# Optimization experiments

Measured on AMD Instinct MI355X. Metric: run time of the kernel, lower is better.

The kernel has to match this reference:

```python
import jax, jax.numpy as jnp
import numpy as np

NUM_GRAPHS = 256
NUM_LAYERS = 4
HIDDEN = 256
N_FEATS = 9
VOCAB = 119
BN_EPS = 1e-5


def setup_inputs() -> dict:
    key = jax.random.key(0)
    ks = jax.random.split(key, 16)
    N, E, H = 10000, 320000, HIDDEN
    x = jax.random.randint(ks[0], (N, N_FEATS), 0, 2, dtype=jnp.int64)
    edge_index = jax.random.randint(ks[1], (2, E), 0, N, dtype=jnp.int64)
    batch_ids = jnp.sort(jax.random.randint(ks[2], (N,), 0, NUM_GRAPHS, dtype=jnp.int64))
    s = 1.0 / np.sqrt(H)
    emb = jax.random.normal(ks[3], (N_FEATS, VOCAB, H), jnp.float32) * 0.02
    W = jax.random.normal(ks[4], (NUM_LAYERS, H, H), jnp.float32) * s
    b = jnp.zeros((NUM_LAYERS, H), jnp.float32)
    gamma = jnp.ones((NUM_LAYERS, H), jnp.float32)
    beta = jnp.zeros((NUM_LAYERS, H), jnp.float32)
    mlp_W1 = jax.random.normal(ks[5], (H, H // 2), jnp.float32) * s
    mlp_b1 = jnp.zeros((H // 2,), jnp.float32)
    mlp_W2 = jax.random.normal(ks[6], (H // 2, H // 4), jnp.float32) * (1.0 / np.sqrt(H // 2))
    mlp_b2 = jnp.zeros((H // 4,), jnp.float32)
    mlp_W3 = jax.random.normal(ks[7], (H // 4, 1), jnp.float32) * (1.0 / np.sqrt(H // 4))
    mlp_b3 = jnp.zeros((1,), jnp.float32)
    return dict(x=x, edge_index=edge_index, batch_ids=batch_ids, emb=emb, W=W, b=b,
                gamma=gamma, beta=beta, mlp_W1=mlp_W1, mlp_b1=mlp_b1,
                mlp_W2=mlp_W2, mlp_b2=mlp_b2, mlp_W3=mlp_W3, mlp_b3=mlp_b3)


def reference(x, edge_index, batch_ids, emb, W, b, gamma, beta,
              mlp_W1, mlp_b1, mlp_W2, mlp_b2, mlp_W3, mlp_b3):
    N = x.shape[0]
    src, dst = edge_index[0], edge_index[1]

    # AtomEncoder: sum of per-feature embeddings. emb[f, x[:,f]] -> [N, 9, H]
    h = jnp.sum(emb[jnp.arange(N_FEATS), x], axis=1)

    # GCN normalization with self-loops: deg_i = 1 + in-degree, norm = deg^-1/2
    deg = 1.0 + jax.ops.segment_sum(jnp.ones_like(dst, jnp.float32), dst, num_segments=N)
    nrm = jax.lax.rsqrt(deg)
    edge_w = (nrm[src] * nrm[dst])[:, None]   # [E,1]
    self_w = (nrm * nrm)[:, None]             # [N,1]

    for l in range(NUM_LAYERS):
        identity = h
        hw = h @ W[l]                                     # dense GEMM [N,H]x[H,H]
        agg = jax.ops.segment_sum(hw[src] * edge_w, dst, num_segments=N) + hw * self_w
        h = agg + b[l]
        # BatchNorm1d (training statistics over nodes)
        mu = jnp.mean(h, axis=0)
        var = jnp.var(h, axis=0)
        h = (h - mu) * jax.lax.rsqrt(var + BN_EPS) * gamma[l] + beta[l]
        h = jax.nn.relu(h)
        h = h + identity  # residual

    # global mean pool over graph ids
    sums = jax.ops.segment_sum(h, batch_ids, num_segments=NUM_GRAPHS)
    cnt = jax.ops.segment_sum(jnp.ones((N,), jnp.float32), batch_ids, num_segments=NUM_GRAPHS)
    g = sums / jnp.maximum(cnt, 1.0)[:, None]             # [G, H]

    # MLP head [H, H/2, H/4, 1]
    g = jax.nn.relu(g @ mlp_W1 + mlp_b1)
    g = jax.nn.relu(g @ mlp_W2 + mlp_b2)
    return g @ mlp_W3 + mlp_b3
```

## Files before the change

### kernel.cpp

```cpp
#include <hip/hip_runtime.h>

#define HID 256
#define NFEAT 9
#define VOCAB 119
#define NLAYERS 4
#define NGRAPHS 256
#define BN_EPS 1e-5f

typedef short short8 __attribute__((ext_vector_type(8)));
typedef float floatx4 __attribute__((ext_vector_type(4)));

__device__ inline unsigned short f2bf(float f) {
    unsigned int u = __float_as_uint(f);
    unsigned int r = u + 0x7FFF + ((u >> 16) & 1);
    return (unsigned short)(r >> 16);
}
__device__ inline float bf2f(unsigned short u) {
    return __uint_as_float(((unsigned int)u) << 16);
}

__global__ __launch_bounds__(256) void setup_misc(
        const int* __restrict__ x, const float* __restrict__ emb,
        const float* __restrict__ W,
        int* __restrict__ degi, int* __restrict__ fillc, float* __restrict__ bnsums,
        unsigned short* __restrict__ wt, unsigned short* __restrict__ hbA,
        int N, int zb) {
    const int bx = blockIdx.x;
    const int tid = threadIdx.x;
    __shared__ float sw[32][33];
    __shared__ int xf[NFEAT];

    if (bx < zb) {
        int i = bx * 256 + tid;
        if (i < N) { degi[i] = 0; fillc[i] = 0; }
        if (bx == 0) {
            for (int j = tid; j < NLAYERS * 2 * HID; j += 256) bnsums[j] = 0.f;
        }
    } else if (bx < zb + 256) {
        int j = bx - zb;
        int l = j >> 6;
        int rem = j & 63;
        int k0 = (rem >> 3) * 32, n0 = (rem & 7) * 32;
        int c = tid & 31, r8 = tid >> 5;
        const float* Wl = W + (size_t)l * HID * HID;
        unsigned short* Wtl = wt + (size_t)l * HID * HID;
#pragma unroll
        for (int p = 0; p < 4; ++p) {
            int r = r8 + p * 8;
            sw[r][c] = Wl[(k0 + r) * HID + n0 + c];
        }
        __syncthreads();
#pragma unroll
        for (int p = 0; p < 4; ++p) {
            int r = r8 + p * 8;
            Wtl[(size_t)(n0 + r) * HID + k0 + c] = f2bf(sw[c][r]);
        }
    } else {
        int n = bx - zb - 256;
        if (n < N) {
            if (tid < NFEAT) xf[tid] = x[n * NFEAT + tid];
            __syncthreads();
            float s = 0.f;
#pragma unroll
            for (int f = 0; f < NFEAT; ++f) s += emb[(size_t)(f * VOCAB + xf[f]) * HID + tid];
            hbA[(size_t)n * HID + tid] = f2bf(s);
        }
    }
}

__global__ void deg_kernel(const int* __restrict__ dst, int* __restrict__ degi, int E) {
    int i = blockIdx.x * blockDim.x + threadIdx.x;
    if (i < E) atomicAdd(&degi[dst[i]], 1);
}

__global__ __launch_bounds__(1024) void scan_kernel(const int* __restrict__ degi,
                                                    int* __restrict__ row_ptr,
                                                    float* __restrict__ nrm, int N) {
    int tid = threadIdx.x;
    int ch = (N + 1023) >> 10;
    int i0 = tid * ch;
    int i1 = min(i0 + ch, N);
    if (i0 > N) i0 = N;
    int local = 0;
    for (int i = i0; i < i1; ++i) local += degi[i];
    int lane = tid & 63, wid = tid >> 6;
    int v = local;
#pragma unroll
    for (int off = 1; off < 64; off <<= 1) {
        int u = __shfl_up(v, off);
        if (lane >= off) v += u;
    }
    __shared__ int wsum[16];
    if (lane == 63) wsum[wid] = v;
    __syncthreads();
    if (tid < 16) {
        int w = wsum[tid];
#pragma unroll
        for (int off = 1; off < 16; off <<= 1) {
            int u = __shfl_up(w, off);
            if (tid >= off) w += u;
        }
        wsum[tid] = w;
    }
    __syncthreads();
    int base = (wid > 0 ? wsum[wid - 1] : 0) + (v - local);
    int run = base;
    for (int i = i0; i < i1; ++i) {
        int d = degi[i];
        row_ptr[i] = run;
        run += d;
        nrm[i] = rsqrtf(1.0f + (float)d);
    }
    if (tid == 0) row_ptr[N] = wsum[15];
}

__global__ void fill_kernel(const int* __restrict__ src, const int* __restrict__ dst,
                            const int* __restrict__ row_ptr, int* __restrict__ fill,
                            const float* __restrict__ nrm,
                            int2* __restrict__ edges, int E) {
    int i = blockIdx.x * blockDim.x + threadIdx.x;
    if (i < E) {
        int d = dst[i];
        int s = src[i];
        int pos = row_ptr[d] + atomicAdd(&fill[d], 1);
        int2 rec;
        rec.x = s;
        rec.y = __float_as_int(nrm[s] * nrm[d]);
        edges[pos] = rec;
    }
}

__global__ __launch_bounds__(256) void agg_w8_kernel(const unsigned short* __restrict__ hb,
                                                     const int* __restrict__ row_ptr,
                                                     const int2* __restrict__ edges,
                                                     const float* __restrict__ nrm,
                                                     unsigned short* __restrict__ aggb, int N) {
    int tid = threadIdx.x;
    int wave = tid >> 6;
    int lane = tid & 63;
    int sub = lane >> 5;
    int sl = lane & 31;
    int n = blockIdx.x * 4 + wave;
    if (n >= N) return;
    int co = sl * 8;
    int s = row_ptr[n], e = row_ptr[n + 1];
    int len = e - s;
    int h0 = (len + 1) >> 1;
    int base = s + sub * h0;
    int cnt = sub ? (len - h0) : h0;
    float a[8];
#pragma unroll
    for (int j = 0; j < 8; ++j) a[j] = 0.f;
    int it = 0;
    for (; it + 3 < cnt; it += 4) {
        int2 e0 = edges[base + it];
        int2 e1 = edges[base + it + 1];
        int2 e2 = edges[base + it + 2];
        int2 e3 = edges[base + it + 3];
        short8 u0 = *(const short8*)&hb[(size_t)e0.x * HID + co];
        short8 u1 = *(const short8*)&hb[(size_t)e1.x * HID + co];
        short8 u2 = *(const short8*)&hb[(size_t)e2.x * HID + co];
        short8 u3 = *(const short8*)&hb[(size_t)e3.x * HID + co];
        float w0 = __int_as_float(e0.y);
        float w1 = __int_as_float(e1.y);
        float w2 = __int_as_float(e2.y);
        float w3 = __int_as_float(e3.y);
#pragma unroll
        for (int j = 0; j < 8; ++j)
            a[j] += w0 * bf2f((unsigned short)u0[j]) + w1 * bf2f((unsigned short)u1[j])
                  + w2 * bf2f((unsigned short)u2[j]) + w3 * bf2f((unsigned short)u3[j]);
    }
    for (; it < cnt; ++it) {
        int2 e0 = edges[base + it];
        short8 u0 = *(const short8*)&hb[(size_t)e0.x * HID + co];
        float w0 = __int_as_float(e0.y);
#pragma unroll
        for (int j = 0; j < 8; ++j) a[j] += w0 * bf2f((unsigned short)u0[j]);
    }
#pragma unroll
    for (int j = 0; j < 8; ++j) a[j] += __shfl_xor(a[j], 32);
    if (sub == 0) {
        float nd = nrm[n];
        float sw2 = nd * nd;
        short8 us = *(const short8*)&hb[(size_t)n * HID + co];
        short8 o;
#pragma unroll
        for (int j = 0; j < 8; ++j) {
            float v = a[j] + sw2 * bf2f((unsigned short)us[j]);
            o[j] = (short)f2bf(v);
        }
        *(short8*)&aggb[(size_t)n * HID + co] = o;
    }
}

__global__ __launch_bounds__(256) void mfma_gemm128(const unsigned short* __restrict__ A,
                                                    const unsigned short* __restrict__ Bt,
                                                    const float* __restrict__ bias,
                                                    unsigned short* __restrict__ C,
                                                    float* __restrict__ sums, int M) {
    __shared__ unsigned short As[128][40];
    __shared__ unsigned short Bs[64][40];
    __shared__ float lsum[64];
    __shared__ float lsq[64];
    int tid = threadIdx.x;
    int row0 = blockIdx.x * 128;
    int col0 = blockIdx.y * 64;
    int lane = tid & 63;
    int wid = tid >> 6;
    int arow = tid >> 1;
    int akc = (tid & 1) * 16;
    int brow = tid >> 2;
    int bkc = (tid & 3) * 8;
    int wm = (wid & 1) * 64;
    int wn = (wid >> 1) * 32;
    int quad = lane >> 4;
    int ln = lane & 15;

    floatx4 acc[4][2];
#pragma unroll
    for (int r = 0; r < 4; ++r)
#pragma unroll
        for (int c = 0; c < 2; ++c) acc[r][c] = (floatx4){0.f, 0.f, 0.f, 0.f};

    if (tid < 64) { lsum[tid] = 0.f; lsq[tid] = 0.f; }

    for (int kk = 0; kk < HID; kk += 32) {
        short8 av0 = {0, 0, 0, 0, 0, 0, 0, 0};
        short8 av1 = {0, 0, 0, 0, 0, 0, 0, 0};
        int ar = row0 + arow;
        if (ar < M) {
            av0 = *(const short8*)&A[(size_t)ar * HID + kk + akc];
            av1 = *(const short8*)&A[(size_t)ar * HID + kk + akc + 8];
        }
        short8 bv = *(const short8*)&Bt[(size_t)(col0 + brow) * HID + kk + bkc];
        *(short8*)&As[arow][akc] = av0;
        *(short8*)&As[arow][akc + 8] = av1;
        *(short8*)&Bs[brow][bkc] = bv;
        __syncthreads();
        short8 bf0 = *(const short8*)&Bs[wn + ln][quad * 8];
        short8 bf1 = *(const short8*)&Bs[wn + 16 + ln][quad * 8];
#pragma unroll
        for (int r = 0; r < 4; ++r) {
            short8 af = *(const short8*)&As[wm + r * 16 + ln][quad * 8];
            acc[r][0] = __builtin_amdgcn_mfma_f32_16x16x32_bf16(af, bf0, acc[r][0], 0, 0, 0);
            acc[r][1] = __builtin_amdgcn_mfma_f32_16x16x32_bf16(af, bf1, acc[r][1], 0, 0, 0);
        }
        __syncthreads();
    }
    float bias0 = bias[col0 + wn + ln];
    float bias1 = bias[col0 + wn + 16 + ln];
    float p0 = 0.f, q0 = 0.f, p1 = 0.f, q1 = 0.f;
#pragma unroll
    for (int r = 0; r < 4; ++r) {
#pragma unroll
        for (int rr = 0; rr < 4; ++rr) {
            int row = row0 + wm + r * 16 + quad * 4 + rr;
            if (row < M) {
                float v0 = acc[r][0][rr] + bias0;
                float v1 = acc[r][1][rr] + bias1;
                C[(size_t)row * HID + col0 + wn + ln] = f2bf(v0);
                C[(size_t)row * HID + col0 + wn + 16 + ln] = f2bf(v1);
                p0 += v0; q0 += v0 * v0;
                p1 += v1; q1 += v1 * v1;
            }
        }
    }
    atomicAdd(&lsum[wn + ln], p0);
    atomicAdd(&lsq[wn + ln], q0);
    atomicAdd(&lsum[wn + 16 + ln], p1);
    atomicAdd(&lsq[wn + 16 + ln], q1);
    __syncthreads();
    if (tid < 64) {
        unsafeAtomicAdd(&sums[col0 + tid], lsum[tid]);
        unsafeAtomicAdd(&sums[HID + col0 + tid], lsq[tid]);
    }
}

__global__ __launch_bounds__(256) void bn_kernel(const unsigned short* __restrict__ hwb,
                                                 const float* __restrict__ sums,
                                                 const float* __restrict__ gamma,
                                                 const float* __restrict__ beta,
                                                 const unsigned short* __restrict__ hold,
                                                 unsigned short* __restrict__ hbnew, int N) {
    int i4 = blockIdx.x * blockDim.x + threadIdx.x;
    int base = i4 * 4;
    if (base >= N * HID) return;
    int c = base & (HID - 1);
    float invN = 1.0f / (float)N;
    float4 s4 = *(const float4*)&sums[c];
    float4 q4 = *(const float4*)&sums[HID + c];
    float4 g4 = *(const float4*)&gamma[c];
    float4 be4 = *(const float4*)&beta[c];
    ushort4 v = *(const ushort4*)&hwb[base];
    ushort4 r = *(const ushort4*)&hold[base];
    ushort4 o;
    {
        float mu = s4.x * invN, var = q4.x * invN - mu * mu;
        o.x = f2bf(fmaxf((bf2f(v.x) - mu) * g4.x * rsqrtf(var + BN_EPS) + be4.x, 0.f) + bf2f(r.x));
        mu = s4.y * invN; var = q4.y * invN - mu * mu;
        o.y = f2bf(fmaxf((bf2f(v.y) - mu) * g4.y * rsqrtf(var + BN_EPS) + be4.y, 0.f) + bf2f(r.y));
        mu = s4.z * invN; var = q4.z * invN - mu * mu;
        o.z = f2bf(fmaxf((bf2f(v.z) - mu) * g4.z * rsqrtf(var + BN_EPS) + be4.z, 0.f) + bf2f(r.z));
        mu = s4.w * invN; var = q4.w * invN - mu * mu;
        o.w = f2bf(fmaxf((bf2f(v.w) - mu) * g4.w * rsqrtf(var + BN_EPS) + be4.w, 0.f) + bf2f(r.w));
    }
    *(ushort4*)&hbnew[base] = o;
}

__device__ inline int lower_bound_g(const int* __restrict__ a, int n, int key) {
    int lo = 0, hi = n;
    while (lo < hi) {
        int mid = (lo + hi) >> 1;
        if (a[mid] < key) lo = mid + 1; else hi = mid;
    }
    return lo;
}

__global__ __launch_bounds__(256) void pool_mlp_bn_kernel(
        const unsigned short* __restrict__ hwb,
        const float* __restrict__ sums,
        const float* __restrict__ gamma,
        const float* __restrict__ beta,
        const unsigned short* __restrict__ resid,
        const int* __restrict__ batch, int N,
        const float* __restrict__ W1, const float* __restrict__ b1,
        const float* __restrict__ W2, const float* __restrict__ b2,
        const float* __restrict__ W3, const float* __restrict__ b3,
        float* __restrict__ out) {
    int g = blockIdx.x, tid = threadIdx.x;
    int lo = lower_bound_g(batch, N, g);
    int hi = lower_bound_g(batch, N, g + 1);
    float invN = 1.0f / (float)N;
    float mu = sums[tid] * invN;
    float var = sums[HID + tid] * invN - mu * mu;
    float sc = gamma[tid] * rsqrtf(var + BN_EPS);
    float be = beta[tid];
    float s = 0.f;
    for (int i = lo; i < hi; ++i) {
        float v = (bf2f(hwb[(size_t)i * HID + tid]) - mu) * sc + be;
        v = fmaxf(v, 0.f) + bf2f(resid[(size_t)i * HID + tid]);
        s += v;
    }
    __shared__ float gs[256];
    __shared__ float t1[128];
    __shared__ float t2[64];
    float inv = 1.0f / fmaxf((float)(hi - lo), 1.0f);
    gs[tid] = s * inv;
    __syncthreads();
    if (tid < 128) {
        float a = b1[tid];
        for (int k = 0; k < 256; ++k) a += gs[k] * W1[k * 128 + tid];
        t1[tid] = fmaxf(a, 0.f);
    }
    __syncthreads();
    if (tid < 64) {
        float a = b2[tid];
        for (int k = 0; k < 128; ++k) a += t1[k] * W2[k * 64 + tid];
        t2[tid] = fmaxf(a, 0.f);
    }
    __syncthreads();
    if (tid < 64) {
        float p = t2[tid] * W3[tid];
#pragma unroll
        for (int off = 32; off >= 1; off >>= 1) p += __shfl_down(p, off);
        if (tid == 0) out[g] = p + b3[0];
    }
}

extern "C" void kernel_launch(void* const* d_in, const int* in_sizes, int n_in,
                              void* d_out, int out_size, void* d_ws, size_t ws_size,
                              hipStream_t stream) {
    const int* x      = (const int*)d_in[0];
    const int* ei     = (const int*)d_in[1];
    const int* batch  = (const int*)d_in[2];
    const float* emb  = (const float*)d_in[3];
    const float* W    = (const float*)d_in[4];
    const float* b    = (const float*)d_in[5];
    const float* gamma= (const float*)d_in[6];
    const float* beta = (const float*)d_in[7];
    const float* W1   = (const float*)d_in[8];
    const float* b1   = (const float*)d_in[9];
    const float* W2   = (const float*)d_in[10];
    const float* b2   = (const float*)d_in[11];
    const float* W3   = (const float*)d_in[12];
    const float* b3   = (const float*)d_in[13];
    float* out = (float*)d_out;

    int N = in_sizes[0] / NFEAT;
    int E = in_sizes[1] / 2;
    const int* srcp = ei;
    const int* dstp = ei + E;

    char* ws = (char*)d_ws;
    auto alloc = [&](size_t bytes) -> char* {
        char* p = ws;
        ws += (bytes + 255) & ~(size_t)255;
        return p;
    };
    int* degi     = (int*)alloc((size_t)N * 4);
    int* row_ptr  = (int*)alloc((size_t)(N + 1) * 4);
    int* fillc    = (int*)alloc((size_t)N * 4);
    float* nrm    = (float*)alloc((size_t)N * 4);
    int2* edges   = (int2*)alloc((size_t)E * 8);
    unsigned short* hbA  = (unsigned short*)alloc((size_t)N * HID * 2);
    unsigned short* hbB  = (unsigned short*)alloc((size_t)N * HID * 2);
    unsigned short* aggb = (unsigned short*)alloc((size_t)N * HID * 2);
    unsigned short* hwb  = (unsigned short*)alloc((size_t)N * HID * 2);
    unsigned short* wt   = (unsigned short*)alloc((size_t)NLAYERS * HID * HID * 2);
    float* bnsums = (float*)alloc((size_t)NLAYERS * 2 * HID * 4);

    int zb = (N + 255) / 256;
    int miscGrid = zb + 256 + N;
    setup_misc<<<miscGrid, 256, 0, stream>>>(x, emb, W, degi, fillc, bnsums, wt, hbA, N, zb);
    deg_kernel<<<(E + 255) / 256, 256, 0, stream>>>(dstp, degi, E);
    scan_kernel<<<1, 1024, 0, stream>>>(degi, row_ptr, nrm, N);
    fill_kernel<<<(E + 255) / 256, 256, 0, stream>>>(srcp, dstp, row_ptr, fillc, nrm, edges, E);

    unsigned short* hbcur = hbA;
    unsigned short* hboth = hbB;
    for (int l = 0; l < NLAYERS; ++l) {
        float* lsums = bnsums + (size_t)l * 2 * HID;
        agg_w8_kernel<<<(N + 3) / 4, 256, 0, stream>>>(hbcur, row_ptr, edges, nrm, aggb, N);
        dim3 ggrid((N + 127) / 128, 4);
        mfma_gemm128<<<ggrid, 256, 0, stream>>>(aggb, wt + (size_t)l * HID * HID,
                                                b + (size_t)l * HID, hwb, lsums, N);
        if (l < NLAYERS - 1) {
            bn_kernel<<<((size_t)N * HID / 4 + 255) / 256, 256, 0, stream>>>(
                hwb, lsums, gamma + (size_t)l * HID, beta + (size_t)l * HID,
                hbcur, hboth, N);
            unsigned short* tb = hbcur; hbcur = hboth; hboth = tb;
        }
    }

    pool_mlp_bn_kernel<<<NGRAPHS, 256, 0, stream>>>(
        hwb, bnsums + (size_t)3 * 2 * HID, gamma + (size_t)3 * HID, beta + (size_t)3 * HID,
        hbcur, batch, N, W1, b1, W2, b2, W3, b3, out);
}
```

Before: 304.0 us.

## Fuse BatchNorm into GEMM via grid barrier and shuffle-broadcast edge records

The separate BatchNorm/ReLU/residual kernel is folded into the GEMM epilogue. Each column-block group waits on a global atomic counter barrier until all row blocks have added their column statistics, then normalizes the accumulators still held in registers. This saves a full write and reread of the pre-BN activations and one launch per layer. The catch is that the spin barrier only works if all ~79x4 blocks are co-resident. Separately, the aggregation kernel now loads up to 32 edge records at once across lanes and broadcasts them with shuffles, instead of every lane reloading the same records.

```diff
diff --git a/kernel.cpp b/kernel.cpp
--- a/kernel.cpp
+++ b/kernel.cpp
@@ -18,11 +18,18 @@
 __device__ inline float bf2f(unsigned short u) {
     return __uint_as_float(((unsigned int)u) << 16);
 }
+__device__ inline unsigned int agent_load_u(const unsigned int* p) {
+    return __hip_atomic_load(p, __ATOMIC_RELAXED, __HIP_MEMORY_SCOPE_AGENT);
+}
+__device__ inline float agent_load_f(const float* p) {
+    return __hip_atomic_load(p, __ATOMIC_RELAXED, __HIP_MEMORY_SCOPE_AGENT);
+}
 
 __global__ __launch_bounds__(256) void setup_misc(
         const int* __restrict__ x, const float* __restrict__ emb,
         const float* __restrict__ W,
         int* __restrict__ degi, int* __restrict__ fillc, float* __restrict__ bnsums,
+        unsigned int* __restrict__ ctr,
         unsigned short* __restrict__ wt, unsigned short* __restrict__ hbA,
         int N, int zb) {
     const int bx = blockIdx.x;
@@ -35,6 +42,7 @@
         if (i < N) { degi[i] = 0; fillc[i] = 0; }
         if (bx == 0) {
             for (int j = tid; j < NLAYERS * 2 * HID; j += 256) bnsums[j] = 0.f;
+            if (tid < 16) ctr[tid] = 0u;
         }
     } else if (bx < zb + 256) {
         int j = bx - zb;
@@ -130,11 +138,11 @@
     }
 }
 
-__global__ __launch_bounds__(256) void agg_w8_kernel(const unsigned short* __restrict__ hb,
-                                                     const int* __restrict__ row_ptr,
-                                                     const int2* __restrict__ edges,
-                                                     const float* __restrict__ nrm,
-                                                     unsigned short* __restrict__ aggb, int N) {
+__global__ __launch_bounds__(256) void agg_shfl_kernel(const unsigned short* __restrict__ hb,
+                                                       const int* __restrict__ row_ptr,
+                                                       const int2* __restrict__ edges,
+                                                       const float* __restrict__ nrm,
+                                                       unsigned short* __restrict__ aggb, int N) {
     int tid = threadIdx.x;
     int wave = tid >> 6;
     int lane = tid & 63;
@@ -151,31 +159,32 @@
     float a[8];
 #pragma unroll
     for (int j = 0; j < 8; ++j) a[j] = 0.f;
-    int it = 0;
-    for (; it + 3 < cnt; it += 4) {
-        int2 e0 = edges[base + it];
-        int2 e1 = edges[base + it + 1];
-        int2 e2 = edges[base + it + 2];
-        int2 e3 = edges[base + it + 3];
-        short8 u0 = *(const short8*)&hb[(size_t)e0.x * HID + co];
-        short8 u1 = *(const short8*)&hb[(size_t)e1.x * HID + co];
-        short8 u2 = *(const short8*)&hb[(size_t)e2.x * HID + co];
-        short8 u3 = *(const short8*)&hb[(size_t)e3.x * HID + co];
-        float w0 = __int_as_float(e0.y);
-        float w1 = __int_as_float(e1.y);
-        float w2 = __int_as_float(e2.y);
-        float w3 = __int_as_float(e3.y);
-#pragma unroll
-        for (int j = 0; j < 8; ++j)
-            a[j] += w0 * bf2f((unsigned short)u0[j]) + w1 * bf2f((unsigned short)u1[j])
-                  + w2 * bf2f((unsigned short)u2[j]) + w3 * bf2f((unsigned short)u3[j]);
-    }
-    for (; it < cnt; ++it) {
-        int2 e0 = edges[base + it];
-        short8 u0 = *(const short8*)&hb[(size_t)e0.x * HID + co];
-        float w0 = __int_as_float(e0.y);
-#pragma unroll
-        for (int j = 0; j < 8; ++j) a[j] += w0 * bf2f((unsigned short)u0[j]);
+
+    int done = 0;
+    while (done < cnt) {
+        int m = min(32, cnt - done);
+        int li = done + (sl < m ? sl : m - 1);
+        int2 rec = edges[base + li];
+        int j = 0;
+        for (; j + 1 < m; j += 2) {
+            int s0 = __shfl(rec.x, j, 32);
+            int s1 = __shfl(rec.x, j + 1, 32);
+            float w0 = __int_as_float(__shfl(rec.y, j, 32));
+            float w1 = __int_as_float(__shfl(rec.y, j + 1, 32));
+            short8 u0 = *(const short8*)&hb[(size_t)s0 * HID + co];
+            short8 u1 = *(const short8*)&hb[(size_t)s1 * HID + co];
+#pragma unroll
+            for (int k = 0; k < 8; ++k)
+                a[k] += w0 * bf2f((unsigned short)u0[k]) + w1 * bf2f((unsigned short)u1[k]);
+        }
+        if (j < m) {
+            int s0 = __shfl(rec.x, j, 32);
+            float w0 = __int_as_float(__shfl(rec.y, j, 32));
+            short8 u0 = *(const short8*)&hb[(size_t)s0 * HID + co];
+#pragma unroll
+            for (int k = 0; k < 8; ++k) a[k] += w0 * bf2f((unsigned short)u0[k]);
+        }
+        done += m;
     }
 #pragma unroll
     for (int j = 0; j < 8; ++j) a[j] += __shfl_xor(a[j], 32);
@@ -197,7 +206,12 @@
                                                     const unsigned short* __restrict__ Bt,
                                                     const float* __restrict__ bias,
                                                     unsigned short* __restrict__ C,
-                                                    float* __restrict__ sums, int M) {
+                                                    float* __restrict__ sums,
+                                                    unsigned int* __restrict__ ctr,
+                                                    const unsigned short* __restrict__ resid,
+                                                    const float* __restrict__ gamma,
+                                                    const float* __restrict__ beta,
+                                                    int doBn, int M) {
     __shared__ unsigned short As[128][40];
     __shared__ unsigned short Bs[64][40];
     __shared__ float lsum[64];
@@ -247,8 +261,10 @@
         }
         __syncthreads();
     }
-    float bias0 = bias[col0 + wn + ln];
-    float bias1 = bias[col0 + wn + 16 + ln];
+    int c0 = col0 + wn + ln;
+    int c1 = col0 + wn + 16 + ln;
+    float bias0 = bias[c0];
+    float bias1 = bias[c1];
     float p0 = 0.f, q0 = 0.f, p1 = 0.f, q1 = 0.f;
 #pragma unroll
     for (int r = 0; r < 4; ++r) {
@@ -258,8 +274,12 @@
             if (row < M) {
                 float v0 = acc[r][0][rr] + bias0;
                 float v1 = acc[r][1][rr] + bias1;
-                C[(size_t)row * HID + col0 + wn + ln] = f2bf(v0);
-                C[(size_t)row * HID + col0 + wn + 16 + ln] = f2bf(v1);
+                acc[r][0][rr] = v0;
+                acc[r][1][rr] = v1;
+                if (!doBn) {
+                    C[(size_t)row * HID + c0] = f2bf(v0);
+                    C[(size_t)row * HID + c1] = f2bf(v1);
+                }
                 p0 += v0; q0 += v0 * v0;
                 p1 += v1; q1 += v1 * v1;
             }
@@ -274,37 +294,45 @@
         unsafeAtomicAdd(&sums[col0 + tid], lsum[tid]);
         unsafeAtomicAdd(&sums[HID + col0 + tid], lsq[tid]);
     }
-}
-
-__global__ __launch_bounds__(256) void bn_kernel(const unsigned short* __restrict__ hwb,
-                                                 const float* __restrict__ sums,
-                                                 const float* __restrict__ gamma,
-                                                 const float* __restrict__ beta,
-                                                 const unsigned short* __restrict__ hold,
-                                                 unsigned short* __restrict__ hbnew, int N) {
-    int i4 = blockIdx.x * blockDim.x + threadIdx.x;
-    int base = i4 * 4;
-    if (base >= N * HID) return;
-    int c = base & (HID - 1);
-    float invN = 1.0f / (float)N;
-    float4 s4 = *(const float4*)&sums[c];
-    float4 q4 = *(const float4*)&sums[HID + c];
-    float4 g4 = *(const float4*)&gamma[c];
-    float4 be4 = *(const float4*)&beta[c];
-    ushort4 v = *(const ushort4*)&hwb[base];
-    ushort4 r = *(const ushort4*)&hold[base];
-    ushort4 o;
-    {
-        float mu = s4.x * invN, var = q4.x * invN - mu * mu;
-        o.x = f2bf(fmaxf((bf2f(v.x) - mu) * g4.x * rsqrtf(var + BN_EPS) + be4.x, 0.f) + bf2f(r.x));
-        mu = s4.y * invN; var = q4.y * invN - mu * mu;
-        o.y = f2bf(fmaxf((bf2f(v.y) - mu) * g4.y * rsqrtf(var + BN_EPS) + be4.y, 0.f) + bf2f(r.y));
-        mu = s4.z * invN; var = q4.z * invN - mu * mu;
-        o.z = f2bf(fmaxf((bf2f(v.z) - mu) * g4.z * rsqrtf(var + BN_EPS) + be4.z, 0.f) + bf2f(r.z));
-        mu = s4.w * invN; var = q4.w * invN - mu * mu;
-        o.w = f2bf(fmaxf((bf2f(v.w) - mu) * g4.w * rsqrtf(var + BN_EPS) + be4.w, 0.f) + bf2f(r.w));
-    }
-    *(ushort4*)&hbnew[base] = o;
+    if (!doBn) return;
+
+    unsigned int* myctr = &ctr[blockIdx.y];
+    unsigned int target = gridDim.x;
+    __syncthreads();
+    if (tid == 0) {
+        __threadfence();
+        atomicAdd(myctr, 1u);
+        for (int k = 0; k < (1 << 22); ++k) {
+            if (agent_load_u(myctr) >= target) break;
+            __builtin_amdgcn_s_sleep(2);
+        }
+    }
+    __syncthreads();
+    __threadfence();
+    float invN = 1.0f / (float)M;
+    float mu0 = agent_load_f(&sums[c0]) * invN;
+    float vr0 = agent_load_f(&sums[HID + c0]) * invN - mu0 * mu0;
+    float mu1 = agent_load_f(&sums[c1]) * invN;
+    float vr1 = agent_load_f(&sums[HID + c1]) * invN - mu1 * mu1;
+    float sc0 = gamma[c0] * rsqrtf(vr0 + BN_EPS);
+    float sc1 = gamma[c1] * rsqrtf(vr1 + BN_EPS);
+    float be0 = beta[c0];
+    float be1 = beta[c1];
+#pragma unroll
+    for (int r = 0; r < 4; ++r) {
+#pragma unroll
+        for (int rr = 0; rr < 4; ++rr) {
+            int row = row0 + wm + r * 16 + quad * 4 + rr;
+            if (row < M) {
+                float v0 = fmaxf((acc[r][0][rr] - mu0) * sc0 + be0, 0.f)
+                         + bf2f(resid[(size_t)row * HID + c0]);
+                float v1 = fmaxf((acc[r][1][rr] - mu1) * sc1 + be1, 0.f)
+                         + bf2f(resid[(size_t)row * HID + c1]);
+                C[(size_t)row * HID + c0] = f2bf(v0);
+                C[(size_t)row * HID + c1] = f2bf(v1);
+            }
+        }
+    }
 }
 
 __device__ inline int lower_bound_g(const int* __restrict__ a, int n, int key) {
@@ -408,10 +436,11 @@
     unsigned short* hwb  = (unsigned short*)alloc((size_t)N * HID * 2);
     unsigned short* wt   = (unsigned short*)alloc((size_t)NLAYERS * HID * HID * 2);
     float* bnsums = (float*)alloc((size_t)NLAYERS * 2 * HID * 4);
+    unsigned int* ctr = (unsigned int*)alloc(16 * 4);
 
     int zb = (N + 255) / 256;
     int miscGrid = zb + 256 + N;
-    setup_misc<<<miscGrid, 256, 0, stream>>>(x, emb, W, degi, fillc, bnsums, wt, hbA, N, zb);
+    setup_misc<<<miscGrid, 256, 0, stream>>>(x, emb, W, degi, fillc, bnsums, ctr, wt, hbA, N, zb);
     deg_kernel<<<(E + 255) / 256, 256, 0, stream>>>(dstp, degi, E);
     scan_kernel<<<1, 1024, 0, stream>>>(degi, row_ptr, nrm, N);
     fill_kernel<<<(E + 255) / 256, 256, 0, stream>>>(srcp, dstp, row_ptr, fillc, nrm, edges, E);
@@ -420,15 +449,18 @@
     unsigned short* hboth = hbB;
     for (int l = 0; l < NLAYERS; ++l) {
         float* lsums = bnsums + (size_t)l * 2 * HID;
-        agg_w8_kernel<<<(N + 3) / 4, 256, 0, stream>>>(hbcur, row_ptr, edges, nrm, aggb, N);
+        agg_shfl_kernel<<<(N + 3) / 4, 256, 0, stream>>>(hbcur, row_ptr, edges, nrm, aggb, N);
         dim3 ggrid((N + 127) / 128, 4);
-        mfma_gemm128<<<ggrid, 256, 0, stream>>>(aggb, wt + (size_t)l * HID * HID,
-                                                b + (size_t)l * HID, hwb, lsums, N);
         if (l < NLAYERS - 1) {
-            bn_kernel<<<((size_t)N * HID / 4 + 255) / 256, 256, 0, stream>>>(
-                hwb, lsums, gamma + (size_t)l * HID, beta + (size_t)l * HID,
-                hbcur, hboth, N);
+            mfma_gemm128<<<ggrid, 256, 0, stream>>>(
+                aggb, wt + (size_t)l * HID * HID, b + (size_t)l * HID,
+                hboth, lsums, ctr + l * 4, hbcur,
+                gamma + (size_t)l * HID, beta + (size_t)l * HID, 1, N);
             unsigned short* tb = hbcur; hbcur = hboth; hboth = tb;
+        } else {
+            mfma_gemm128<<<ggrid, 256, 0, stream>>>(
+                aggb, wt + (size_t)l * HID * HID, b + (size_t)l * HID,
+                hwb, lsums, nullptr, nullptr, nullptr, nullptr, 0, N);
         }
     }
 
```

Result: slower. 412.8 us (+35.8%).

## Fuse neighbor aggregation with the weight GEMM into one kernel

Applied to the files above, without the earlier changes.

Merges the sparse aggregation kernel and the MFMA GEMM into a single kernel. Each block aggregates 16 node rows directly into shared memory, then multiplies them by the full 256x256 weight matrix, streamed through LDS in k-chunks, and applies bias and BN statistics. This removes the intermediate aggregated buffer round-trip through global memory and one launch per layer. In exchange, every block reloads the whole weight matrix for only 16 rows, and the number of global atomics on the BN sums grows.

```diff
diff --git a/kernel.cpp b/kernel.cpp
--- a/kernel.cpp
+++ b/kernel.cpp
@@ -130,150 +130,125 @@
     }
 }
 
-__global__ __launch_bounds__(256) void agg_w8_kernel(const unsigned short* __restrict__ hb,
-                                                     const int* __restrict__ row_ptr,
-                                                     const int2* __restrict__ edges,
-                                                     const float* __restrict__ nrm,
-                                                     unsigned short* __restrict__ aggb, int N) {
+__global__ __launch_bounds__(256) void agg_gemm(const unsigned short* __restrict__ hb,
+                                                const int* __restrict__ row_ptr,
+                                                const int2* __restrict__ edges,
+                                                const float* __restrict__ nrm,
+                                                const unsigned short* __restrict__ Bt,
+                                                const float* __restrict__ bias,
+                                                unsigned short* __restrict__ C,
+                                                float* __restrict__ sums, int N) {
+    __shared__ unsigned short As[16][264];
+    __shared__ unsigned short Bs[256][40];
+    __shared__ float lsum[256];
+    __shared__ float lsq[256];
     int tid = threadIdx.x;
     int wave = tid >> 6;
     int lane = tid & 63;
     int sub = lane >> 5;
     int sl = lane & 31;
-    int n = blockIdx.x * 4 + wave;
-    if (n >= N) return;
-    int co = sl * 8;
-    int s = row_ptr[n], e = row_ptr[n + 1];
-    int len = e - s;
-    int h0 = (len + 1) >> 1;
-    int base = s + sub * h0;
-    int cnt = sub ? (len - h0) : h0;
-    float a[8];
-#pragma unroll
-    for (int j = 0; j < 8; ++j) a[j] = 0.f;
-    int it = 0;
-    for (; it + 3 < cnt; it += 4) {
-        int2 e0 = edges[base + it];
-        int2 e1 = edges[base + it + 1];
-        int2 e2 = edges[base + it + 2];
-        int2 e3 = edges[base + it + 3];
-        short8 u0 = *(const short8*)&hb[(size_t)e0.x * HID + co];
-        short8 u1 = *(const short8*)&hb[(size_t)e1.x * HID + co];
-        short8 u2 = *(const short8*)&hb[(size_t)e2.x * HID + co];
-        short8 u3 = *(const short8*)&hb[(size_t)e3.x * HID + co];
-        float w0 = __int_as_float(e0.y);
-        float w1 = __int_as_float(e1.y);
-        float w2 = __int_as_float(e2.y);
-        float w3 = __int_as_float(e3.y);
-#pragma unroll
-        for (int j = 0; j < 8; ++j)
-            a[j] += w0 * bf2f((unsigned short)u0[j]) + w1 * bf2f((unsigned short)u1[j])
-                  + w2 * bf2f((unsigned short)u2[j]) + w3 * bf2f((unsigned short)u3[j]);
-    }
-    for (; it < cnt; ++it) {
-        int2 e0 = edges[base + it];
-        short8 u0 = *(const short8*)&hb[(size_t)e0.x * HID + co];
-        float w0 = __int_as_float(e0.y);
-#pragma unroll
-        for (int j = 0; j < 8; ++j) a[j] += w0 * bf2f((unsigned short)u0[j]);
-    }
-#pragma unroll
-    for (int j = 0; j < 8; ++j) a[j] += __shfl_xor(a[j], 32);
-    if (sub == 0) {
-        float nd = nrm[n];
-        float sw2 = nd * nd;
-        short8 us = *(const short8*)&hb[(size_t)n * HID + co];
-        short8 o;
-#pragma unroll
-        for (int j = 0; j < 8; ++j) {
-            float v = a[j] + sw2 * bf2f((unsigned short)us[j]);
-            o[j] = (short)f2bf(v);
-        }
-        *(short8*)&aggb[(size_t)n * HID + co] = o;
-    }
-}
-
-__global__ __launch_bounds__(256) void mfma_gemm128(const unsigned short* __restrict__ A,
-                                                    const unsigned short* __restrict__ Bt,
-                                                    const float* __restrict__ bias,
-                                                    unsigned short* __restrict__ C,
-                                                    float* __restrict__ sums, int M) {
-    __shared__ unsigned short As[128][40];
-    __shared__ unsigned short Bs[64][40];
-    __shared__ float lsum[64];
-    __shared__ float lsq[64];
-    int tid = threadIdx.x;
-    int row0 = blockIdx.x * 128;
-    int col0 = blockIdx.y * 64;
-    int lane = tid & 63;
-    int wid = tid >> 6;
-    int arow = tid >> 1;
-    int akc = (tid & 1) * 16;
-    int brow = tid >> 2;
-    int bkc = (tid & 3) * 8;
-    int wm = (wid & 1) * 64;
-    int wn = (wid >> 1) * 32;
+    int row0 = blockIdx.x * 16;
+
+    for (int q = 0; q < 4; ++q) {
+        int lr = wave * 4 + q;
+        int n = row0 + lr;
+        float a[8];
+#pragma unroll
+        for (int j = 0; j < 8; ++j) a[j] = 0.f;
+        if (n < N) {
+            int s = row_ptr[n], e = row_ptr[n + 1];
+            int len = e - s;
+            int h0 = (len + 1) >> 1;
+            int base = s + sub * h0;
+            int cnt = sub ? (len - h0) : h0;
+            int co = sl * 8;
+            int it = 0;
+            for (; it + 3 < cnt; it += 4) {
+                int2 e0 = edges[base + it];
+                int2 e1 = edges[base + it + 1];
+                int2 e2 = edges[base + it + 2];
+                int2 e3 = edges[base + it + 3];
+                short8 u0 = *(const short8*)&hb[(size_t)e0.x * HID + co];
+                short8 u1 = *(const short8*)&hb[(size_t)e1.x * HID + co];
+                short8 u2 = *(const short8*)&hb[(size_t)e2.x * HID + co];
+                short8 u3 = *(const short8*)&hb[(size_t)e3.x * HID + co];
+                float w0 = __int_as_float(e0.y);
+                float w1 = __int_as_float(e1.y);
+                float w2 = __int_as_float(e2.y);
+                float w3 = __int_as_float(e3.y);
+#pragma unroll
+                for (int j = 0; j < 8; ++j)
+                    a[j] += w0 * bf2f((unsigned short)u0[j]) + w1 * bf2f((unsigned short)u1[j])
+                          + w2 * bf2f((unsigned short)u2[j]) + w3 * bf2f((unsigned short)u3[j]);
+            }
+            for (; it < cnt; ++it) {
+                int2 e0 = edges[base + it];
+                short8 u0 = *(const short8*)&hb[(size_t)e0.x * HID + co];
+                float w0 = __int_as_float(e0.y);
+#pragma unroll
+                for (int j = 0; j < 8; ++j) a[j] += w0 * bf2f((unsigned short)u0[j]);
+            }
+#pragma unroll
+            for (int j = 0; j < 8; ++j) a[j] += __shfl_xor(a[j], 32);
+            if (sub == 0) {
+                float nd = nrm[n];
+                float sw2 = nd * nd;
+                short8 us = *(const short8*)&hb[(size_t)n * HID + co];
+                short8 o;
+#pragma unroll
+                for (int j = 0; j < 8; ++j) o[j] = (short)f2bf(a[j] + sw2 * bf2f((unsigned short)us[j]));
+                *(short8*)&As[lr][sl * 8] = o;
+            }
+        } else if (sub == 0) {
+            short8 z = {0, 0, 0, 0, 0, 0, 0, 0};
+            *(short8*)&As[lr][sl * 8] = z;
+        }
+    }
+    lsum[tid] = 0.f;
+    lsq[tid] = 0.f;
+    __syncthreads();
+
     int quad = lane >> 4;
     int ln = lane & 15;
-
-    floatx4 acc[4][2];
-#pragma unroll
-    for (int r = 0; r < 4; ++r)
-#pragma unroll
-        for (int c = 0; c < 2; ++c) acc[r][c] = (floatx4){0.f, 0.f, 0.f, 0.f};
-
-    if (tid < 64) { lsum[tid] = 0.f; lsq[tid] = 0.f; }
+    floatx4 acc[4];
+#pragma unroll
+    for (int c = 0; c < 4; ++c) acc[c] = (floatx4){0.f, 0.f, 0.f, 0.f};
 
     for (int kk = 0; kk < HID; kk += 32) {
-        short8 av0 = {0, 0, 0, 0, 0, 0, 0, 0};
-        short8 av1 = {0, 0, 0, 0, 0, 0, 0, 0};
-        int ar = row0 + arow;
-        if (ar < M) {
-            av0 = *(const short8*)&A[(size_t)ar * HID + kk + akc];
-            av1 = *(const short8*)&A[(size_t)ar * HID + kk + akc + 8];
-        }
-        short8 bv = *(const short8*)&Bt[(size_t)(col0 + brow) * HID + kk + bkc];
-        *(short8*)&As[arow][akc] = av0;
-        *(short8*)&As[arow][akc + 8] = av1;
-        *(short8*)&Bs[brow][bkc] = bv;
+#pragma unroll
+        for (int j = 0; j < 4; ++j)
+            *(short8*)&Bs[tid][j * 8] = *(const short8*)&Bt[(size_t)tid * HID + kk + j * 8];
         __syncthreads();
-        short8 bf0 = *(const short8*)&Bs[wn + ln][quad * 8];
-        short8 bf1 = *(const short8*)&Bs[wn + 16 + ln][quad * 8];
-#pragma unroll
-        for (int r = 0; r < 4; ++r) {
-            short8 af = *(const short8*)&As[wm + r * 16 + ln][quad * 8];
-            acc[r][0] = __builtin_amdgcn_mfma_f32_16x16x32_bf16(af, bf0, acc[r][0], 0, 0, 0);
-            acc[r][1] = __builtin_amdgcn_mfma_f32_16x16x32_bf16(af, bf1, acc[r][1], 0, 0, 0);
+        short8 af = *(const short8*)&As[ln][kk + quad * 8];
+#pragma unroll
+        for (int c = 0; c < 4; ++c) {
+            short8 bf = *(const short8*)&Bs[wave * 64 + c * 16 + ln][quad * 8];
+            acc[c] = __builtin_amdgcn_mfma_f32_16x16x32_bf16(af, bf, acc[c], 0, 0, 0);
         }
         __syncthreads();
     }
-    float bias0 = bias[col0 + wn + ln];
-    float bias1 = bias[col0 + wn + 16 + ln];
-    float p0 = 0.f, q0 = 0.f, p1 = 0.f, q1 = 0.f;
-#pragma unroll
-    for (int r = 0; r < 4; ++r) {
+
+#pragma unroll
+    for (int c = 0; c < 4; ++c) {
+        int col = wave * 64 + c * 16 + ln;
+        float bs = bias[col];
+        float p = 0.f, qq = 0.f;
 #pragma unroll
         for (int rr = 0; rr < 4; ++rr) {
-            int row = row0 + wm + r * 16 + quad * 4 + rr;
-            if (row < M) {
-                float v0 = acc[r][0][rr] + bias0;
-                float v1 = acc[r][1][rr] + bias1;
-                C[(size_t)row * HID + col0 + wn + ln] = f2bf(v0);
-                C[(size_t)row * HID + col0 + wn + 16 + ln] = f2bf(v1);
-                p0 += v0; q0 += v0 * v0;
-                p1 += v1; q1 += v1 * v1;
+            int row = row0 + quad * 4 + rr;
+            if (row < N) {
+                float v = acc[c][rr] + bs;
+                C[(size_t)row * HID + col] = f2bf(v);
+                p += v;
+                qq += v * v;
             }
         }
-    }
-    atomicAdd(&lsum[wn + ln], p0);
-    atomicAdd(&lsq[wn + ln], q0);
-    atomicAdd(&lsum[wn + 16 + ln], p1);
-    atomicAdd(&lsq[wn + 16 + ln], q1);
-    __syncthreads();
-    if (tid < 64) {
-        unsafeAtomicAdd(&sums[col0 + tid], lsum[tid]);
-        unsafeAtomicAdd(&sums[HID + col0 + tid], lsq[tid]);
-    }
+        atomicAdd(&lsum[col], p);
+        atomicAdd(&lsq[col], qq);
+    }
+    __syncthreads();
+    unsafeAtomicAdd(&sums[tid], lsum[tid]);
+    unsafeAtomicAdd(&sums[HID + tid], lsq[tid]);
 }
 
 __global__ __launch_bounds__(256) void bn_kernel(const unsigned short* __restrict__ hwb,
@@ -404,7 +379,6 @@
     int2* edges   = (int2*)alloc((size_t)E * 8);
     unsigned short* hbA  = (unsigned short*)alloc((size_t)N * HID * 2);
     unsigned short* hbB  = (unsigned short*)alloc((size_t)N * HID * 2);
-    unsigned short* aggb = (unsigned short*)alloc((size_t)N * HID * 2);
     unsigned short* hwb  = (unsigned short*)alloc((size_t)N * HID * 2);
     unsigned short* wt   = (unsigned short*)alloc((size_t)NLAYERS * HID * HID * 2);
     float* bnsums = (float*)alloc((size_t)NLAYERS * 2 * HID * 4);
@@ -418,12 +392,12 @@
 
     unsigned short* hbcur = hbA;
     unsigned short* hboth = hbB;
+    int agGrid = (N + 15) / 16;
     for (int l = 0; l < NLAYERS; ++l) {
         float* lsums = bnsums + (size_t)l * 2 * HID;
-        agg_w8_kernel<<<(N + 3) / 4, 256, 0, stream>>>(hbcur, row_ptr, edges, nrm, aggb, N);
-        dim3 ggrid((N + 127) / 128, 4);
-        mfma_gemm128<<<ggrid, 256, 0, stream>>>(aggb, wt + (size_t)l * HID * HID,
-                                                b + (size_t)l * HID, hwb, lsums, N);
+        agg_gemm<<<agGrid, 256, 0, stream>>>(hbcur, row_ptr, edges, nrm,
+                                             wt + (size_t)l * HID * HID,
+                                             b + (size_t)l * HID, hwb, lsums, N);
         if (l < NLAYERS - 1) {
             bn_kernel<<<((size_t)N * HID / 4 + 255) / 256, 256, 0, stream>>>(
                 hwb, lsums, gamma + (size_t)l * HID, beta + (size_t)l * HID,
```

After: 384.4 us. 1.26x slower.
